# Performance work log

Measured on AMD Instinct MI355X. Metric: run time of the kernel, lower is better.

Reference implementation:

```python
import jax, jax.numpy as jnp
import numpy as np

N_HEAD = 4
GROUPS = 4
EPS = 1e-5


def group_norm(x, w, b):
    # x: [B, C, D, H, W], normalized over (C//GROUPS, D, H, W) per group
    B, C = x.shape[0], x.shape[1]
    xr = x.reshape(B, GROUPS, -1)
    mu = xr.mean(axis=2, keepdims=True)
    var = xr.var(axis=2, keepdims=True)
    xn = ((xr - mu) * jax.lax.rsqrt(var + EPS)).reshape(x.shape)
    return xn * w.reshape(1, C, 1, 1, 1) + b.reshape(1, C, 1, 1, 1)


def conv3d(x, w, b, pad):
    y = jax.lax.conv_general_dilated(
        x, w, window_strides=(1, 1, 1), padding=[(pad, pad)] * 3,
        dimension_numbers=('NCDHW', 'OIDHW', 'NCDHW'))
    return y + b.reshape(1, -1, 1, 1, 1)


def upsample_nearest(x, size):
    # torch nearest: out index i maps to floor(i * in / out)
    out = x
    for ax in (2, 3, 4):
        n_in = out.shape[ax]
        idx = (jnp.arange(size) * n_in) // size
        out = jnp.take(out, idx, axis=ax)
    return out


def setup_inputs() -> dict:
    key = jax.random.key(0)
    ks = jax.random.split(key, 8)
    B, C, D, H, W = 2, 256, 32, 32, 32
    inp = {
        'q': jax.random.normal(ks[0], (B, C, D, H, W), jnp.float32),
        'k': jax.random.normal(ks[1], (B, C, D, H, W), jnp.float32),
        'v': jax.random.normal(ks[2], (B, C, D, H, W), jnp.float32),
        'gn_w': jnp.ones((C,), jnp.float32),
        'gn_b': jnp.zeros((C,), jnp.float32),
        'out_w': jax.random.normal(ks[3], (C, C, 1, 1, 1), jnp.float32) * 0.02,
        'out_b': jnp.zeros((C,), jnp.float32),
        'dg_w': jax.random.normal(ks[4], (3, C, 3, 3, 3), jnp.float32) * 0.02,
        'dg_b': jnp.zeros((3,), jnp.float32),
        'nl_w': jax.random.normal(ks[5], (3, 3, 3, 3, 3), jnp.float32) * 0.02,
        'nl_b': jnp.zeros((3,), jnp.float32),
        'size': 64,
    }
    return inp


def reference(q, k, v, gn_w, gn_b, out_w, out_b, dg_w, dg_b, nl_w, nl_b, size):
    B, C, D, H, W = q.shape
    c = C // N_HEAD
    n = D * H * W
    residual = q
    nq = group_norm(q, gn_w, gn_b)
    nk = group_norm(k, gn_w, gn_b)
    nv = group_norm(v, gn_w, gn_b)
    qh = nq.reshape(B, N_HEAD, c, n)
    kh = jax.nn.softmax(nk.reshape(B, N_HEAD, c, n), axis=-1)
    vh = nv.reshape(B, N_HEAD, c, n)
    # linear attention: context over spatial tokens, then project q
    context = jnp.einsum('bhdn,bhen->bhde', kh, vh)      # [B,H,c,c]
    out = jnp.einsum('bhde,bhdn->bhen', context, qh)     # [B,H,c,n]
    out = out.reshape(B, C, D, H, W)
    out = conv3d(out, out_w, out_b, pad=0)
    out = conv3d(out + residual, dg_w, dg_b, pad=1)      # [B,3,D,H,W]
    out = upsample_nearest(out, size)                    # [B,3,size,size,size]
    out = conv3d(out, nl_w, nl_b, pad=1)
    return out
```

## Files before the change

### kernel.cpp

```cpp
#include <hip/hip_runtime.h>
#include <math.h>

typedef unsigned int uint32;
typedef unsigned short u16;

typedef __bf16 bf16x8 __attribute__((ext_vector_type(8)));
typedef float f32x4 __attribute__((ext_vector_type(4)));

#define OFF_STATS 0
#define OFF_MUSR  64
#define OFF_L     128
#define OFF_MROW  640
#define OFF_MAXV  1280
#define OFF_MINV  1792
#define OFF_CTX   2048
#define OFF_MBT   34816
#define OFF_KB    165888
#define OFF_Z     167936
#define OFF_DG    8556544
#define OFF_CTXP  8753152
#define OFF_LP    10850304
#define OFF_DGP   8753152
#define WS_PART_FLOATS 15044608

__device__ __forceinline__ float bf2f(u16 h){ return __uint_as_float(((uint32)h)<<16); }
__device__ __forceinline__ u16 f2bf(float f){ uint32 u=__float_as_uint(f); return (u16)((u + 0x7fffu + ((u>>16)&1u))>>16); }

__global__ __launch_bounds__(512) void k_stats(const float* __restrict__ k,
                                               const float* __restrict__ v, float* __restrict__ ws){
  int gid8 = blockIdx.x >> 6;
  int chunk = blockIdx.x & 63;
  int gid = 8 + gid8;
  const float* src = (gid8 < 8)? k : v;
  int bg = gid8 & 7;
  const float* base = src + (size_t)bg*2097152 + (size_t)chunk*32768;
  int tid = threadIdx.x;
  float s=0.f, ss=0.f;
  #pragma unroll
  for (int it=0; it<8; ++it){
    float4 x = *(const float4*)(base + it*4096 + tid*8);
    float4 y = *(const float4*)(base + it*4096 + tid*8 + 4);
    s += ((x.x+x.y)+(x.z+x.w)) + ((y.x+y.y)+(y.z+y.w));
    ss = fmaf(x.x,x.x, fmaf(x.y,x.y, fmaf(x.z,x.z, fmaf(x.w,x.w, ss))));
    ss = fmaf(y.x,y.x, fmaf(y.y,y.y, fmaf(y.z,y.z, fmaf(y.w,y.w, ss))));
  }
  for (int o=32;o>0;o>>=1){
    s  += __shfl_down(s,o);  ss += __shfl_down(ss,o);
  }
  __shared__ float rsum[8], rssq[8];
  int w = tid>>6;
  if ((tid&63)==0){ rsum[w]=s; rssq[w]=ss; }
  __syncthreads();
  if (tid==0){
    float fs = ((rsum[0]+rsum[1])+(rsum[2]+rsum[3])) + ((rsum[4]+rsum[5])+(rsum[6]+rsum[7]));
    float fq = ((rssq[0]+rssq[1])+(rssq[2]+rssq[3])) + ((rssq[4]+rssq[5])+(rssq[6]+rssq[7]));
    atomicAdd(&ws[OFF_STATS + gid*2],   fs);
    atomicAdd(&ws[OFF_STATS + gid*2+1], fq);
  }
}

__global__ void k_finalize(float* __restrict__ ws){
  int tid = threadIdx.x;
  if (tid >= 8 && tid < 24){
    float s=ws[OFF_STATS+2*tid], ss=ws[OFF_STATS+2*tid+1];
    const float inv = 1.f/2097152.f;
    float mu = s*inv;
    float var = ss*inv - mu*mu;
    ws[OFF_MUSR+2*tid]=mu; ws[OFF_MUSR+2*tid+1]=rsqrtf(var+1e-5f);
  }
}

__device__ __forceinline__ float4 expaff(float4 x, float a, float b, float& s){
  float4 e;
  e.x=__expf(fmaf(x.x,a,b)); e.y=__expf(fmaf(x.y,a,b));
  e.z=__expf(fmaf(x.z,a,b)); e.w=__expf(fmaf(x.w,a,b));
  s += (e.x+e.y)+(e.z+e.w);
  return e;
}
__device__ __forceinline__ float4 aff4(float4 x, float a, float b){
  return make_float4(fmaf(x.x,a,b), fmaf(x.y,a,b), fmaf(x.z,a,b), fmaf(x.w,a,b));
}
__device__ __forceinline__ bf16x8 cvt8(float4 a, float4 b){
  bf16x8 r;
  r[0]=(__bf16)a.x; r[1]=(__bf16)a.y; r[2]=(__bf16)a.z; r[3]=(__bf16)a.w;
  r[4]=(__bf16)b.x; r[5]=(__bf16)b.y; r[6]=(__bf16)b.z; r[7]=(__bf16)b.w;
  return r;
}

__global__ __launch_bounds__(256) void k_ctx(const float* __restrict__ qq,
                                             const float* __restrict__ kk, const float* __restrict__ vv,
                                             const float* __restrict__ gw, const float* __restrict__ gb,
                                             float* __restrict__ ws, int usePart){
  int tid = threadIdx.x;
  if (blockIdx.y >= 8){
    int sblk = (blockIdx.y - 8)*64 + blockIdx.x;
    int row0 = sblk*2;
    int half = tid>>7, l = tid&127;
    const float* p = qq + (size_t)(row0+half)*32768 + l*4;
    float s=0.f, ss=0.f;
    #pragma unroll 8
    for (int it=0; it<64; ++it){
      float4 x = *(const float4*)(p + it*512);
      s += (x.x+x.y)+(x.z+x.w);
      ss = fmaf(x.x,x.x, fmaf(x.y,x.y, fmaf(x.z,x.z, fmaf(x.w,x.w, ss))));
    }
    for (int o=32;o>0;o>>=1){ s += __shfl_down(s,o); ss += __shfl_down(ss,o); }
    __shared__ float rs_[4], rq_[4];
    if ((tid&63)==0){ rs_[tid>>6]=s; rq_[tid>>6]=ss; }
    __syncthreads();
    if (tid==0){
      int gid = (row0>>8)*4 + ((row0>>6)&3);
      atomicAdd(&ws[OFF_STATS + 2*gid],   (rs_[0]+rs_[1])+(rs_[2]+rs_[3]));
      atomicAdd(&ws[OFF_STATS + 2*gid+1], (rq_[0]+rq_[1])+(rq_[2]+rq_[3]));
    }
    return;
  }

  int chunk = blockIdx.x;
  int bh = blockIdx.y; int b=bh>>2, h=bh&3;
  int lane = tid & 63, wv = tid >> 6;
  int m16 = lane & 15, quad = lane >> 4;
  int dhalf = wv >> 1, ehalf = wv & 1;

  int gik = 8+bh, giv = 16+bh;
  float muk=ws[OFF_MUSR+2*gik], rsk=ws[OFF_MUSR+2*gik+1];
  float muv=ws[OFF_MUSR+2*giv], rsv=ws[OFF_MUSR+2*giv+1];
  float akr[2], bmkr[2], avr[2], bvvr[2];
  #pragma unroll
  for (int t=0;t<2;++t){
    int c = h*64 + dhalf*32 + t*16 + m16;
    float a = rsk*gw[c];
    akr[t]=a; bmkr[t]=gb[c]-muk*a;
  }
  #pragma unroll
  for (int t=0;t<2;++t){
    int c = h*64 + ehalf*32 + t*16 + m16;
    float a = rsv*gw[c];
    avr[t]=a; bvvr[t]=gb[c]-muv*a;
  }

  const float* kb = kk + (size_t)b*8388608 + (size_t)h*2097152;
  const float* vb = vv + (size_t)b*8388608 + (size_t)h*2097152;
  int nb0 = chunk*512;
  const float* kp[2]; const float* vp[2];
  kp[0] = kb + (size_t)(dhalf*32 + m16)*32768 + nb0 + quad*8;
  kp[1] = kp[0] + (size_t)16*32768;
  vp[0] = vb + (size_t)(ehalf*32 + m16)*32768 + nb0 + quad*8;
  vp[1] = vp[0] + (size_t)16*32768;

  f32x4 acc[2][2];
  #pragma unroll
  for (int i=0;i<2;++i){
    #pragma unroll
    for (int j=0;j<2;++j) acc[i][j] = 0.f;
  }
  float lsum[2] = {0.f, 0.f};

#define KCTX_LOAD(DK, DV, OFFS) do { \
    _Pragma("unroll") \
    for (int t=0;t<2;++t){ \
      DK[t][0] = *(const float4*)(kp[t] + (OFFS)); \
      DK[t][1] = *(const float4*)(kp[t] + (OFFS) + 4); \
      DV[t][0] = *(const float4*)(vp[t] + (OFFS)); \
      DV[t][1] = *(const float4*)(vp[t] + (OFFS) + 4); \
    } } while(0)

#define KCTX_STEP(SK, SV) do { \
    bf16x8 afr[2], bfr[2]; \
    _Pragma("unroll") \
    for (int t=0;t<2;++t){ \
      float4 e0 = expaff(SK[t][0], akr[t], bmkr[t], lsum[t]); \
      float4 e1 = expaff(SK[t][1], akr[t], bmkr[t], lsum[t]); \
      afr[t] = cvt8(e0,e1); \
      float4 v0 = aff4(SV[t][0], avr[t], bvvr[t]); \
      float4 v1 = aff4(SV[t][1], avr[t], bvvr[t]); \
      bfr[t] = cvt8(v0,v1); \
    } \
    _Pragma("unroll") \
    for (int i=0;i<2;++i){ \
      _Pragma("unroll") \
      for (int j=0;j<2;++j) \
        acc[i][j] = __builtin_amdgcn_mfma_f32_16x16x32_bf16(afr[i], bfr[j], acc[i][j], 0, 0, 0); \
    } } while(0)

  float4 ka[2][2], va[2][2];
  KCTX_LOAD(ka, va, 0);
  for (int s=0; s<15; ++s){
    float4 kn[2][2], vn[2][2];
    KCTX_LOAD(kn, vn, (s+1)*32);
    KCTX_STEP(ka, va);
    #pragma unroll
    for (int t=0;t<2;++t){
      ka[t][0]=kn[t][0]; ka[t][1]=kn[t][1];
      va[t][0]=vn[t][0]; va[t][1]=vn[t][1];
    }
  }
  KCTX_STEP(ka, va);
#undef KCTX_LOAD
#undef KCTX_STEP

  #pragma unroll
  for (int t=0;t<2;++t){
    lsum[t] += __shfl_down(lsum[t], 16);
    lsum[t] += __shfl_down(lsum[t], 32);
  }

  if (usePart){
    float* cp = ws + OFF_CTXP + (size_t)(chunk*8+bh)*4096;
    #pragma unroll
    for (int i=0;i<2;++i){
      #pragma unroll
      for (int j=0;j<2;++j){
        int row0 = dhalf*32 + i*16 + quad*4;
        int col  = ehalf*32 + j*16 + m16;
        #pragma unroll
        for (int r=0;r<4;++r)
          cp[(row0+r)*64 + col] = acc[i][j][r];
      }
    }
    if (ehalf==0 && quad==0){
      #pragma unroll
      for (int t=0;t<2;++t)
        ws[OFF_LP + (chunk*8+bh)*64 + dhalf*32 + t*16 + m16] = lsum[t];
    }
  } else {
    float* cp = ws + OFF_CTX + (size_t)bh*4096;
    #pragma unroll
    for (int i=0;i<2;++i){
      #pragma unroll
      for (int j=0;j<2;++j){
        int row0 = dhalf*32 + i*16 + quad*4;
        int col  = ehalf*32 + j*16 + m16;
        #pragma unroll
        for (int r=0;r<4;++r)
          atomicAdd(&cp[(row0+r)*64 + col], acc[i][j][r]);
      }
    }
    if (ehalf==0 && quad==0){
      #pragma unroll
      for (int t=0;t<2;++t)
        atomicAdd(&ws[OFF_L + bh*64 + dhalf*32 + t*16 + m16], lsum[t]);
    }
  }
}

__global__ void k_ctxred(float* __restrict__ ws){
  int i = blockIdx.x*256 + threadIdx.x;
  if (i < 32768){
    float s = 0.f;
    const float* p = ws + OFF_CTXP + i;
    #pragma unroll 8
    for (int c=0;c<64;++c) s += p[(size_t)c*32768];
    ws[OFF_CTX + i] = s;
  } else if (i < 33280){
    int j = i - 32768;
    float s=0.f; const float* p = ws + OFF_LP + j;
    #pragma unroll 8
    for (int c=0;c<64;++c) s += p[c*512];
    ws[OFF_L + j] = s;
  }
}

__global__ __launch_bounds__(256) void k_weff(const float* __restrict__ w1, const float* __restrict__ ob,
                                              const float* __restrict__ gw, const float* __restrict__ gb,
                                              float* __restrict__ ws){
  int co = blockIdx.x; int b = blockIdx.y;
  int cp = threadIdx.x;
  int hp = cp>>6, dp = cp&63;
  const float* ctx = ws + OFF_CTX + (size_t)(b*4+hp)*4096 + dp*64;
  const float* w1p = w1 + co*256 + hp*64;
  float s = 0.f;
  #pragma unroll 8
  for (int e=0;e<64;++e) s = fmaf(w1p[e], ctx[e], s);
  float L = ws[OFF_L + b*256 + cp];
  float weff = s / L;
  int gi = b*4 + hp;
  float sq_  = ws[OFF_STATS + 2*gi];
  float sqq_ = ws[OFF_STATS + 2*gi + 1];
  const float invN = 1.f/2097152.f;
  float mu = sq_*invN;
  float rs = rsqrtf(sqq_*invN - mu*mu + 1e-5f);
  float aq = rs*gw[cp]; float bq = gb[cp] - mu*aq;
  u16* mbp = (u16*)(ws + OFF_MBT);
  mbp[(size_t)b*65536 + (size_t)co*256 + cp] = f2bf(weff*aq);
  float kp = weff*bq;
  for (int o=32;o>0;o>>=1) kp += __shfl_down(kp,o);
  __shared__ float red[4];
  if ((cp&63)==0) red[cp>>6]=kp;
  __syncthreads();
  if (cp==0) ws[OFF_KB + b*256 + co] = ob[co] + ((red[0]+red[1])+(red[2]+red[3]));
}

__global__ __launch_bounds__(256, 4) void k_z(const float* __restrict__ q, float* __restrict__ ws){
  extern __shared__ char smem[];
  u16* As = (u16*)smem;
  u16* Bs = As + 128*72;
  u16* Cs = (u16*)smem;
  int nt = blockIdx.x, cot = blockIdx.y, b = blockIdx.z;
  int n0 = nt*128, co0 = cot*128;
  int tid = threadIdx.x;
  int lane = tid & 63, wv = tid >> 6;
  int m16 = lane & 15, quad = lane >> 4;
  int wco = (wv>>1)*64, wn = (wv&1)*64;
  const u16* mb = (const u16*)(ws + OFF_MBT) + (size_t)b*65536;
  const float* qb = q + (size_t)b*8388608;
  f32x4 acc[4][4];
  #pragma unroll
  for (int i=0;i<4;++i){
    #pragma unroll
    for (int j=0;j<4;++j) acc[i][j] = 0.f;
  }
  int r2 = tid>>1, seg = tid&1;
  int nq = tid & 31, cp0 = tid >> 5;
  for (int kt=0; kt<4; ++kt){
    {
      const u16* src = mb + (size_t)(co0 + r2)*256 + kt*64 + seg*32;
      u16* dst = As + r2*72 + seg*32;
      uint4 w0 = *(const uint4*)(src);
      uint4 w1 = *(const uint4*)(src+8);
      uint4 w2 = *(const uint4*)(src+16);
      uint4 w3 = *(const uint4*)(src+24);
      *(uint4*)(dst)    = w0; *(uint4*)(dst+8)  = w1;
      *(uint4*)(dst+16) = w2; *(uint4*)(dst+24) = w3;
    }
    #pragma unroll
    for (int p=0;p<4;++p){
      int cpair = cp0 + 8*p;
      int c = kt*64 + 2*cpair;
      const float* q0 = qb + (size_t)c*32768 + n0 + nq;
      const float* q1 = q0 + 32768;
      #pragma unroll
      for (int i=0;i<4;++i){
        float a  = q0[32*i];
        float bb = q1[32*i];
        uint32 dw = (uint32)f2bf(a) | ((uint32)f2bf(bb)<<16);
        *(uint32*)(Bs + (nq+32*i)*72 + 2*cpair) = dw;
      }
    }
    __syncthreads();
    #pragma unroll
    for (int ks=0; ks<2; ++ks){
      bf16x8 af[4], bfr[4];
      #pragma unroll
      for (int i=0;i<4;++i) af[i]  = *(const bf16x8*)(As + (wco + i*16 + m16)*72 + ks*32 + quad*8);
      #pragma unroll
      for (int j=0;j<4;++j) bfr[j] = *(const bf16x8*)(Bs + (wn + j*16 + m16)*72 + ks*32 + quad*8);
      #pragma unroll
      for (int i=0;i<4;++i){
        #pragma unroll
        for (int j=0;j<4;++j)
          acc[i][j] = __builtin_amdgcn_mfma_f32_16x16x32_bf16(af[i], bfr[j], acc[i][j], 0, 0, 0);
      }
    }
    __syncthreads();
  }
  #pragma unroll
  for (int i=0;i<4;++i){
    #pragma unroll
    for (int r=0;r<4;++r){
      int row = wco + i*16 + quad*4 + r;
      #pragma unroll
      for (int j=0;j<4;++j)
        Cs[row*136 + wn + j*16 + m16] = f2bf(acc[i][j][r]);
    }
  }
  __syncthreads();
  {
    int co = co0 + r2;
    float kbv = ws[OFF_KB + b*256 + co];
    u16* zp = (u16*)(ws + OFF_Z) + (size_t)b*8388608 + (size_t)co*32768 + n0 + seg*64;
    const float* qr = qb + (size_t)co*32768 + n0 + seg*64;
    #pragma unroll
    for (int ch=0; ch<8; ++ch){
      uint4 cv = *(const uint4*)(Cs + r2*136 + seg*64 + ch*8);
      float4 qa = *(const float4*)(qr + ch*8);
      float4 qc = *(const float4*)(qr + ch*8 + 4);
      float z0 = qa.x + bf2f((u16)(cv.x&0xffff)) + kbv;
      float z1 = qa.y + bf2f((u16)(cv.x>>16))    + kbv;
      float z2 = qa.z + bf2f((u16)(cv.y&0xffff)) + kbv;
      float z3 = qa.w + bf2f((u16)(cv.y>>16))    + kbv;
      float z4 = qc.x + bf2f((u16)(cv.z&0xffff)) + kbv;
      float z5 = qc.y + bf2f((u16)(cv.z>>16))    + kbv;
      float z6 = qc.z + bf2f((u16)(cv.w&0xffff)) + kbv;
      float z7 = qc.w + bf2f((u16)(cv.w>>16))    + kbv;
      uint4 u;
      u.x = (uint32)f2bf(z0) | ((uint32)f2bf(z1)<<16);
      u.y = (uint32)f2bf(z2) | ((uint32)f2bf(z3)<<16);
      u.z = (uint32)f2bf(z4) | ((uint32)f2bf(z5)<<16);
      u.w = (uint32)f2bf(z6) | ((uint32)f2bf(z7)<<16);
      *(uint4*)(zp + ch*8) = u;
    }
  }
}

__global__ __launch_bounds__(256) void k_dg(const float* __restrict__ dgw, float* __restrict__ ws, int usePart){
  int tile = blockIdx.x;
  int split = blockIdx.y;
  int b = blockIdx.z;
  int d0 = (tile>>1)*8, h0=(tile&1)*16;
  int tid = threadIdx.x;
  int wt = tid&1, hy=(tid>>1)&15, dx=tid>>5;
  int d = d0+dx, h = h0+hy, w0 = wt*16;
  int cbeg = split*4;
  __shared__ float wss[4][27][4];
  for (int i=tid;i<432;i+=256){
    int ci = i/108; int r = i - ci*108; int tap = r>>2; int o = r&3;
    wss[ci][tap][o] = (o<3)? dgw[o*6912 + (cbeg+ci)*27 + tap] : 0.f;
  }
  __syncthreads();
  const u16* zp = (const u16*)(ws+OFF_Z) + (size_t)b*8388608;
  float acc[3][16];
  #pragma unroll
  for (int o=0;o<3;++o){
    #pragma unroll
    for (int j=0;j<16;++j) acc[o][j]=0.f;
  }
  for (int ci=0; ci<4; ++ci){
    const u16* zc = zp + (size_t)(cbeg+ci)*32768;
    #pragma unroll
    for (int kd=0;kd<3;++kd){
      int gd = d+kd-1;
      #pragma unroll
      for (int kh=0;kh<3;++kh){
        int gh = h+kh-1;
        bool rv = (gd>=0) & (gd<32) & (gh>=0) & (gh<32);
        const u16* rowp = zc + gd*1024 + gh*32 + w0;
        uint4 u0 = *(const uint4*)(rowp);
        uint4 u1 = *(const uint4*)(rowp+8);
        u16 le = (wt==0)? (u16)0 : rowp[-1];
        u16 ri = (wt==1)? (u16)0 : rowp[16];
        if (!rv){ u0 = make_uint4(0,0,0,0); u1 = make_uint4(0,0,0,0); le = 0; ri = 0; }
        float r[18];
        r[0]  = bf2f(le);
        r[1]  = bf2f((u16)(u0.x&0xffff)); r[2]  = bf2f((u16)(u0.x>>16));
        r[3]  = bf2f((u16)(u0.y&0xffff)); r[4]  = bf2f((u16)(u0.y>>16));
        r[5]  = bf2f((u16)(u0.z&0xffff)); r[6]  = bf2f((u16)(u0.z>>16));
        r[7]  = bf2f((u16)(u0.w&0xffff)); r[8]  = bf2f((u16)(u0.w>>16));
        r[9]  = bf2f((u16)(u1.x&0xffff)); r[10] = bf2f((u16)(u1.x>>16));
        r[11] = bf2f((u16)(u1.y&0xffff)); r[12] = bf2f((u16)(u1.y>>16));
        r[13] = bf2f((u16)(u1.z&0xffff)); r[14] = bf2f((u16)(u1.z>>16));
        r[15] = bf2f((u16)(u1.w&0xffff)); r[16] = bf2f((u16)(u1.w>>16));
        r[17] = bf2f(ri);
        #pragma unroll
        for (int kw=0;kw<3;++kw){
          float4 wv = *(const float4*)&wss[ci][kd*9+kh*3+kw][0];
          #pragma unroll
          for (int j=0;j<16;++j){
            acc[0][j]=fmaf(r[j+kw],wv.x,acc[0][j]);
            acc[1][j]=fmaf(r[j+kw],wv.y,acc[1][j]);
            acc[2][j]=fmaf(r[j+kw],wv.z,acc[2][j]);
          }
        }
      }
    }
  }
  if (usePart){
    u16* op = (u16*)(ws + OFF_DGP) + (size_t)split*196608 + (size_t)b*98304;
    #pragma unroll
    for (int o=0;o<3;++o){
      int base = o*32768 + d*1024 + h*32 + w0;
      uint4 p0, p1;
      p0.x = (uint32)f2bf(acc[o][0])  | ((uint32)f2bf(acc[o][1])<<16);
      p0.y = (uint32)f2bf(acc[o][2])  | ((uint32)f2bf(acc[o][3])<<16);
      p0.z = (uint32)f2bf(acc[o][4])  | ((uint32)f2bf(acc[o][5])<<16);
      p0.w = (uint32)f2bf(acc[o][6])  | ((uint32)f2bf(acc[o][7])<<16);
      p1.x = (uint32)f2bf(acc[o][8])  | ((uint32)f2bf(acc[o][9])<<16);
      p1.y = (uint32)f2bf(acc[o][10]) | ((uint32)f2bf(acc[o][11])<<16);
      p1.z = (uint32)f2bf(acc[o][12]) | ((uint32)f2bf(acc[o][13])<<16);
      p1.w = (uint32)f2bf(acc[o][14]) | ((uint32)f2bf(acc[o][15])<<16);
      *(uint4*)(op + base)     = p0;
      *(uint4*)(op + base + 8) = p1;
    }
  } else {
    float* op = ws + OFF_DG + (size_t)b*98304;
    #pragma unroll
    for (int o=0;o<3;++o){
      #pragma unroll
      for (int j=0;j<16;++j)
        atomicAdd(&op[o*32768 + d*1024 + h*32 + w0 + j], acc[o][j]);
    }
  }
}

__global__ void k_dgred(float* __restrict__ ws){
  int i = blockIdx.x*256 + threadIdx.x;
  float s = 0.f;
  const u16* p = (const u16*)(ws + OFF_DGP) + i;
  #pragma unroll 8
  for (int c=0;c<64;++c) s += bf2f(p[(size_t)c*196608]);
  ws[OFF_DG + i] = s;
}

__global__ __launch_bounds__(256) void k_up(const float* __restrict__ dgb, const float* __restrict__ nlw,
                                            const float* __restrict__ nlb, const float* __restrict__ ws,
                                            float* __restrict__ out){
  int b = blockIdx.y; int tileIdx = blockIdx.x;
  int zt0 = (tileIdx&7)*8, yt0 = ((tileIdx>>3)&7)*8, xt0 = (tileIdx>>6)*4;
  int sx0 = (xt0>>1)-1, sy0 = (yt0>>1)-1, sz0 = (zt0>>1)-1;
  __shared__ float ds[3][4][6][6];
  __shared__ float wl[243];
  const float* dgp = ws + OFF_DG + (size_t)b*98304;
  for (int i=threadIdx.x; i<432; i+=256){
    int ch = i/144; int r = i-ch*144; int sx=r/36; int rr=r-sx*36; int sy=rr/6; int sz=rr-sy*6;
    int gx = sx0+sx, gy = sy0+sy, gz = sz0+sz;
    float v=0.f;
    if (gx>=0&&gx<32&&gy>=0&&gy<32&&gz>=0&&gz<32) v = dgp[ch*32768 + gx*1024 + gy*32 + gz] + dgb[ch];
    ds[ch][sx][sy][sz] = v;
  }
  for (int i=threadIdx.x;i<243;i+=256) wl[i] = nlw[i];
  __syncthreads();
  int zt = threadIdx.x&7, yt=(threadIdx.x>>3)&7, xt=threadIdx.x>>6;
  int x = xt0+xt, y=yt0+yt, zc=zt0+zt;
  float a0=nlb[0], a1=nlb[1], a2=nlb[2];
  #pragma unroll
  for (int i=0;i<3;++i){
    #pragma unroll
    for (int kd=0;kd<3;++kd){
      int sxi = ((x+kd-1)>>1) - sx0;
      #pragma unroll
      for (int kh=0;kh<3;++kh){
        int syi = ((y+kh-1)>>1) - sy0;
        #pragma unroll
        for (int kw=0;kw<3;++kw){
          int szi = ((zc+kw-1)>>1) - sz0;
          float vv = ds[i][sxi][syi][szi];
          int tap = kd*9+kh*3+kw;
          a0 = fmaf(vv, wl[i*27+tap],      a0);
          a1 = fmaf(vv, wl[81+i*27+tap],   a1);
          a2 = fmaf(vv, wl[162+i*27+tap],  a2);
        }
      }
    }
  }
  size_t o0 = (size_t)b*786432 + (size_t)x*4096 + y*64 + zc;
  out[o0] = a0; out[o0+262144] = a1; out[o0+524288] = a2;
}

extern "C" void kernel_launch(void* const* d_in, const int* in_sizes, int n_in,
                              void* d_out, int out_size, void* d_ws, size_t ws_size,
                              hipStream_t stream){
  const float* q    = (const float*)d_in[0];
  const float* k    = (const float*)d_in[1];
  const float* v    = (const float*)d_in[2];
  const float* gnw  = (const float*)d_in[3];
  const float* gnb  = (const float*)d_in[4];
  const float* outw = (const float*)d_in[5];
  const float* outb = (const float*)d_in[6];
  const float* dgw  = (const float*)d_in[7];
  const float* dgb  = (const float*)d_in[8];
  const float* nlw  = (const float*)d_in[9];
  const float* nlb  = (const float*)d_in[10];
  float* out = (float*)d_out;
  float* ws  = (float*)d_ws;
  int usePart = (ws_size >= (size_t)WS_PART_FLOATS*4) ? 1 : 0;

  (void)hipMemsetAsync(ws, 0, 139264, stream);
  (void)hipMemsetAsync((void*)(ws + OFF_DG), 0, 196608*4, stream);

  k_stats   <<<dim3(1024),   dim3(512), 0, stream>>>(k,v,ws);
  k_finalize<<<dim3(1),      dim3(32),  0, stream>>>(ws);
  k_ctx     <<<dim3(64,12),  dim3(256), 0, stream>>>(q,k,v,gnw,gnb,ws,usePart);
  if (usePart) k_ctxred<<<dim3(130), dim3(256), 0, stream>>>(ws);
  k_weff    <<<dim3(256,2),  dim3(256), 0, stream>>>(outw,outb,gnw,gnb,ws);
  k_z       <<<dim3(256,2,2),dim3(256), 36864, stream>>>(q,ws);
  k_dg      <<<dim3(8,64,2), dim3(256), 0, stream>>>(dgw,ws,usePart);
  if (usePart) k_dgred<<<dim3(768), dim3(256), 0, stream>>>(ws);
  k_up      <<<dim3(1024,2), dim3(256), 0, stream>>>(dgb,nlw,nlb,ws,out);
}
```

Before: 383.1 us.

## Double-buffer q tile in k_z and read weight fragments directly from global

```diff
diff --git a/kernel.cpp b/kernel.cpp
--- a/kernel.cpp
+++ b/kernel.cpp
@@ -293,8 +293,7 @@
 
 __global__ __launch_bounds__(256, 4) void k_z(const float* __restrict__ q, float* __restrict__ ws){
   extern __shared__ char smem[];
-  u16* As = (u16*)smem;
-  u16* Bs = As + 128*72;
+  u16* Bs = (u16*)smem;
   u16* Cs = (u16*)smem;
   int nt = blockIdx.x, cot = blockIdx.y, b = blockIdx.z;
   int n0 = nt*128, co0 = cot*128;
@@ -312,39 +311,37 @@
   }
   int r2 = tid>>1, seg = tid&1;
   int nq = tid & 31, cp0 = tid >> 5;
+
+#define KZ_STAGE(BUF, KT) do { \
+    _Pragma("unroll") \
+    for (int p=0;p<4;++p){ \
+      int cpair = cp0 + 8*p; \
+      int c = (KT)*64 + 2*cpair; \
+      const float* q0 = qb + (size_t)c*32768 + n0 + nq; \
+      const float* q1 = q0 + 32768; \
+      _Pragma("unroll") \
+      for (int i=0;i<4;++i){ \
+        float a  = q0[32*i]; \
+        float bb = q1[32*i]; \
+        uint32 dw = (uint32)f2bf(a) | ((uint32)f2bf(bb)<<16); \
+        *(uint32*)(Bs + (BUF)*9216 + (nq+32*i)*72 + 2*cpair) = dw; \
+      } \
+    } } while(0)
+
+  KZ_STAGE(0, 0);
+  __syncthreads();
   for (int kt=0; kt<4; ++kt){
-    {
-      const u16* src = mb + (size_t)(co0 + r2)*256 + kt*64 + seg*32;
-      u16* dst = As + r2*72 + seg*32;
-      uint4 w0 = *(const uint4*)(src);
-      uint4 w1 = *(const uint4*)(src+8);
-      uint4 w2 = *(const uint4*)(src+16);
-      uint4 w3 = *(const uint4*)(src+24);
-      *(uint4*)(dst)    = w0; *(uint4*)(dst+8)  = w1;
-      *(uint4*)(dst+16) = w2; *(uint4*)(dst+24) = w3;
-    }
-    #pragma unroll
-    for (int p=0;p<4;++p){
-      int cpair = cp0 + 8*p;
-      int c = kt*64 + 2*cpair;
-      const float* q0 = qb + (size_t)c*32768 + n0 + nq;
-      const float* q1 = q0 + 32768;
-      #pragma unroll
-      for (int i=0;i<4;++i){
-        float a  = q0[32*i];
-        float bb = q1[32*i];
-        uint32 dw = (uint32)f2bf(a) | ((uint32)f2bf(bb)<<16);
-        *(uint32*)(Bs + (nq+32*i)*72 + 2*cpair) = dw;
-      }
-    }
-    __syncthreads();
+    int buf = kt & 1;
+    if (kt < 3) KZ_STAGE(buf^1, kt+1);
     #pragma unroll
     for (int ks=0; ks<2; ++ks){
       bf16x8 af[4], bfr[4];
       #pragma unroll
-      for (int i=0;i<4;++i) af[i]  = *(const bf16x8*)(As + (wco + i*16 + m16)*72 + ks*32 + quad*8);
-      #pragma unroll
-      for (int j=0;j<4;++j) bfr[j] = *(const bf16x8*)(Bs + (wn + j*16 + m16)*72 + ks*32 + quad*8);
+      for (int i=0;i<4;++i)
+        af[i] = *(const bf16x8*)(mb + (size_t)(co0 + wco + i*16 + m16)*256 + kt*64 + ks*32 + quad*8);
+      #pragma unroll
+      for (int j=0;j<4;++j)
+        bfr[j] = *(const bf16x8*)(Bs + buf*9216 + (wn + j*16 + m16)*72 + ks*32 + quad*8);
       #pragma unroll
       for (int i=0;i<4;++i){
         #pragma unroll
@@ -354,6 +351,8 @@
     }
     __syncthreads();
   }
+#undef KZ_STAGE
+
   #pragma unroll
   for (int i=0;i<4;++i){
     #pragma unroll
```

Measured after the change: 374.6 us. 1.02x faster.
